# Kernel optimization log

Measured on AMD Instinct MI355X. Metric: run time of the kernel, lower is better.

## Reference

```python
import jax, jax.numpy as jnp
import numpy as np
from jax import lax

D = 512
K = 5
HID = 2 * D
EPS = 1e-5


def layernorm(x, g, b):
    mu = jnp.mean(x, axis=-1, keepdims=True)
    var = jnp.mean((x - mu) ** 2, axis=-1, keepdims=True)
    return (x - mu) * lax.rsqrt(var + EPS) * g + b


def setup_inputs() -> dict:
    key = jax.random.key(0)
    ks = jax.random.split(key, 16)
    B, T = 8, 4096
    sc = lambda fan: 1.0 / np.sqrt(fan)
    return {
        "x": jax.random.normal(ks[0], (B, T, D), jnp.float32),
        "decay_logit": jnp.zeros((D,), jnp.float32),
        "W_out": jax.random.uniform(ks[1], (D, D), jnp.float32, -sc(D), sc(D)),
        "b_out": jax.random.uniform(ks[2], (D,), jnp.float32, -sc(D), sc(D)),
        "conv_w": jax.random.uniform(ks[3], (D, 1, K), jnp.float32, -sc(K), sc(K)),
        "conv_b": jax.random.uniform(ks[4], (D,), jnp.float32, -sc(K), sc(K)),
        "ln1_g": jnp.ones((D,), jnp.float32),
        "ln1_b": jnp.zeros((D,), jnp.float32),
        "ln2_g": jnp.ones((D,), jnp.float32),
        "ln2_b": jnp.zeros((D,), jnp.float32),
        "W1": jax.random.uniform(ks[5], (HID, D), jnp.float32, -sc(D), sc(D)),
        "b1": jax.random.uniform(ks[6], (HID,), jnp.float32, -sc(D), sc(D)),
        "W2": jax.random.uniform(ks[7], (D, HID), jnp.float32, -sc(HID), sc(HID)),
        "b2": jax.random.uniform(ks[8], (D,), jnp.float32, -sc(HID), sc(HID)),
    }


def retention_core(xn, decay_logit, W_out, b_out, conv_w, conv_b):
    # xn: [B, T, D]
    B, T, _ = xn.shape
    a = jax.nn.sigmoid(decay_logit)  # [D]

    def step(s, xt):  # s, xt: [B, D]
        s = a * s + (1.0 - a) * xt
        return s, s

    s0 = jnp.zeros((B, D), xn.dtype)
    _, ss = lax.scan(step, s0, jnp.swapaxes(xn, 0, 1))  # [T, B, D]
    ss = jnp.swapaxes(ss, 0, 1)  # [B, T, D]
    y_ret = jnp.einsum("btd,ed->bte", ss, W_out) + b_out

    # depthwise conv1d, 'same' padding (K odd)
    xc = jnp.swapaxes(xn, 1, 2)  # [B, D, T]
    pad = (K - 1) // 2
    y_loc = lax.conv_general_dilated(
        xc, conv_w, window_strides=(1,), padding=[(pad, pad)],
        feature_group_count=D, dimension_numbers=("NCH", "OIH", "NCH"))
    y_loc = jnp.swapaxes(y_loc + conv_b[None, :, None], 1, 2)  # [B, T, D]
    return y_ret + y_loc


def reference(x, decay_logit, W_out, b_out, conv_w, conv_b,
              ln1_g, ln1_b, ln2_g, ln2_b, W1, b1, W2, b2):
    y = retention_core(layernorm(x, ln1_g, ln1_b),
                       decay_logit, W_out, b_out, conv_w, conv_b)
    x = x + y
    h = layernorm(x, ln2_g, ln2_b)
    h = jax.nn.gelu(jnp.einsum("btd,hd->bth", h, W1) + b1, approximate=False)
    y = jnp.einsum("bth,dh->btd", h, W2) + b2
    return x + y
```

## Files before the change

### kernel.cpp

```cpp
#include <hip/hip_runtime.h>
#include <stdint.h>

typedef unsigned short u16;

#define DIM 512
#define HIDN 1024
#define TT 4096
#define BB 8
#define MM 32768
#define CH 128
#define CL 32

__device__ __forceinline__ u16 f2bf(float f) {
  union { float f; uint32_t u; } v; v.f = f;
  uint32_t u = v.u;
  uint32_t r = u + 0x7fffu + ((u >> 16) & 1u);
  return (u16)(r >> 16);
}
__device__ __forceinline__ float bf2f(u16 h) {
  union { uint32_t u; float f; } v; v.u = ((uint32_t)h) << 16; return v.f;
}

typedef __bf16 bf16x8 __attribute__((ext_vector_type(8)));
typedef float f32x4 __attribute__((ext_vector_type(4)));

__global__ __launch_bounds__(256) void prep_kernel(
    const float* __restrict__ wout, const float* __restrict__ w1,
    const float* __restrict__ w2, const float* __restrict__ dl,
    const float* __restrict__ convw,
    u16* __restrict__ wout_h, u16* __restrict__ w1_h, u16* __restrict__ w2_h,
    float* __restrict__ a, float* __restrict__ oma, float* __restrict__ aL,
    float* __restrict__ convwT) {
  int i = blockIdx.x * 256 + threadIdx.x;
  if (i < DIM * DIM) wout_h[i] = f2bf(wout[i]);
  if (i < HIDN * DIM) { w1_h[i] = f2bf(w1[i]); w2_h[i] = f2bf(w2[i]); }
  if (i < 5 * DIM) {
    int kk = i / DIM, n = i - kk * DIM;
    convwT[i] = convw[n * 5 + kk];
  }
  if (i < DIM) {
    float av = 1.0f / (1.0f + expf(-dl[i]));
    a[i] = av; oma[i] = 1.0f - av; aL[i] = powf(av, (float)CL);
  }
}

__global__ __launch_bounds__(256) void ln_rows(
    const float* __restrict__ xin, const float* __restrict__ g,
    const float* __restrict__ bvec, u16* __restrict__ out) {
  int lane = threadIdx.x & 63, wave = threadIdx.x >> 6;
  size_t row = (size_t)blockIdx.x * 4 + wave;
  const float4* xr = (const float4*)(xin + row * DIM);
  float4 v0 = xr[lane * 2 + 0];
  float4 v1 = xr[lane * 2 + 1];
  float s1 = v0.x + v0.y + v0.z + v0.w + v1.x + v1.y + v1.z + v1.w;
  float s2 = v0.x * v0.x + v0.y * v0.y + v0.z * v0.z + v0.w * v0.w
           + v1.x * v1.x + v1.y * v1.y + v1.z * v1.z + v1.w * v1.w;
#pragma unroll
  for (int o = 1; o < 64; o <<= 1) { s1 += __shfl_xor(s1, o); s2 += __shfl_xor(s2, o); }
  float mu = s1 * (1.0f / DIM);
  float var = s2 * (1.0f / DIM) - mu * mu;
  float rs = rsqrtf(var + 1e-5f);
  const float4* gr = (const float4*)g;
  const float4* br = (const float4*)bvec;
  float4 g0 = gr[lane * 2], g1 = gr[lane * 2 + 1];
  float4 b0 = br[lane * 2], b1 = br[lane * 2 + 1];
  uint32_t p0 = (uint32_t)f2bf((v0.x - mu) * rs * g0.x + b0.x) | ((uint32_t)f2bf((v0.y - mu) * rs * g0.y + b0.y) << 16);
  uint32_t p1 = (uint32_t)f2bf((v0.z - mu) * rs * g0.z + b0.z) | ((uint32_t)f2bf((v0.w - mu) * rs * g0.w + b0.w) << 16);
  uint32_t p2 = (uint32_t)f2bf((v1.x - mu) * rs * g1.x + b1.x) | ((uint32_t)f2bf((v1.y - mu) * rs * g1.y + b1.y) << 16);
  uint32_t p3 = (uint32_t)f2bf((v1.z - mu) * rs * g1.z + b1.z) | ((uint32_t)f2bf((v1.w - mu) * rs * g1.w + b1.w) << 16);
  uint4 pk; pk.x = p0; pk.y = p1; pk.z = p2; pk.w = p3;
  ((uint4*)(out + row * DIM))[lane] = pk;
}

__global__ __launch_bounds__(256) void scan_local(
    const u16* __restrict__ xn, const float* __restrict__ a,
    const float* __restrict__ oma, float* __restrict__ carry) {
  int idx = blockIdx.x * 256 + threadIdx.x;
  int d = idx & (DIM - 1);
  int c = (idx >> 9) & (CH - 1);
  int b = idx >> 16;
  float av = a[d], om = oma[d];
  const u16* xp = xn + ((size_t)(b * TT + c * CL)) * DIM + d;
  float s = 0.f;
#pragma unroll
  for (int i = 0; i < CL; ++i)
    s = fmaf(av, s, om * bf2f(xp[(size_t)i * DIM]));
  carry[((size_t)(b * CH + c)) * DIM + d] = s;
}

__global__ __launch_bounds__(256) void scan_carry(
    const float* __restrict__ carry, const float* __restrict__ aL,
    float* __restrict__ start) {
  int idx = blockIdx.x * 256 + threadIdx.x;
  int d = idx & (DIM - 1);
  int b = idx >> 9;
  float al = aL[d];
  float s = 0.f;
#pragma unroll 8
  for (int c = 0; c < CH; ++c) {
    size_t o = ((size_t)(b * CH + c)) * DIM + d;
    start[o] = s;
    s = fmaf(al, s, carry[o]);
  }
}

__global__ __launch_bounds__(256) void scan_emit(
    const u16* __restrict__ xn, const float* __restrict__ a,
    const float* __restrict__ oma, const float* __restrict__ start,
    u16* __restrict__ ss) {
  int idx = blockIdx.x * 256 + threadIdx.x;
  int d = idx & (DIM - 1);
  int c = (idx >> 9) & (CH - 1);
  int b = idx >> 16;
  float av = a[d], om = oma[d];
  const u16* xp = xn + ((size_t)(b * TT + c * CL)) * DIM + d;
  u16* sp = ss + ((size_t)(b * TT + c * CL)) * DIM + d;
  float s = start[((size_t)(b * CH + c)) * DIM + d];
#pragma unroll
  for (int i = 0; i < CL; ++i) {
    s = fmaf(av, s, om * bf2f(xp[(size_t)i * DIM]));
    sp[(size_t)i * DIM] = f2bf(s);
  }
}

template <int Kd, int EPI>
__global__ __launch_bounds__(256) void gemm_bt(
    const u16* __restrict__ A, const u16* __restrict__ Bmat,
    const float* __restrict__ bias, const float* __restrict__ resid,
    const u16* __restrict__ xn, const float* __restrict__ convwT,
    const float* __restrict__ convb, float* __restrict__ outf,
    u16* __restrict__ outh) {
  __shared__ alignas(16) u16 sA[128 * 64];
  __shared__ alignas(16) u16 sB[128 * 64];
  const int tid = threadIdx.x;
  const int lane = tid & 63, wave = tid >> 6;
  const int wr = (wave >> 1) * 64, wc = (wave & 1) * 64;
  const int rA = lane & 15, q = lane >> 4;

  f32x4 acc[4][4];
#pragma unroll
  for (int i = 0; i < 4; i++)
#pragma unroll
    for (int j = 0; j < 4; j++) acc[i][j] = (f32x4){0.f, 0.f, 0.f, 0.f};

  const size_t rowTile = (size_t)blockIdx.y * 128;
  const size_t colTile = (size_t)blockIdx.x * 128;
  const u16* Abase = A + rowTile * Kd;
  const u16* Bbase = Bmat + colTile * Kd;

  const int lrow = lane >> 3;
  const int lslot = lane & 7;
  const int gk = ((lslot ^ lrow) & 7) * 8;

  for (int kt = 0; kt < Kd; kt += 64) {
    __syncthreads();
#pragma unroll
    for (int it = 0; it < 4; ++it) {
      const int m0 = (it * 4 + wave) * 8;
      const u16* ga = Abase + (size_t)(m0 + lrow) * Kd + kt + gk;
      const u16* gb = Bbase + (size_t)(m0 + lrow) * Kd + kt + gk;
      __builtin_amdgcn_global_load_lds(
          (const __attribute__((address_space(1))) void*)ga,
          (__attribute__((address_space(3))) void*)&sA[m0 * 64], 16, 0, 0);
      __builtin_amdgcn_global_load_lds(
          (const __attribute__((address_space(1))) void*)gb,
          (__attribute__((address_space(3))) void*)&sB[m0 * 64], 16, 0, 0);
    }
    __syncthreads();
#pragma unroll
    for (int ks = 0; ks < 2; ++ks) {
      bf16x8 af[4], bfr[4];
#pragma unroll
      for (int mi = 0; mi < 4; ++mi) {
        int r = wr + mi * 16 + rA;
        int pos = ((ks * 4 + q) ^ (r & 7));
        af[mi] = *(const bf16x8*)&sA[r * 64 + pos * 8];
      }
#pragma unroll
      for (int ni = 0; ni < 4; ++ni) {
        int r = wc + ni * 16 + rA;
        int pos = ((ks * 4 + q) ^ (r & 7));
        bfr[ni] = *(const bf16x8*)&sB[r * 64 + pos * 8];
      }
#pragma unroll
      for (int mi = 0; mi < 4; ++mi)
#pragma unroll
        for (int ni = 0; ni < 4; ++ni)
          acc[mi][ni] = __builtin_amdgcn_mfma_f32_16x16x32_bf16(bfr[ni], af[mi], acc[mi][ni], 0, 0, 0);
    }
  }

#pragma unroll
  for (int mi = 0; mi < 4; ++mi) {
    size_t m = rowTile + wr + mi * 16 + rA;
#pragma unroll
    for (int ni = 0; ni < 4; ++ni) {
      int n0 = (int)colTile + wc + ni * 16 + q * 4;
      f32x4 v = acc[mi][ni];
      float4 bv = *(const float4*)&bias[n0];
      float val0 = v[0] + bv.x, val1 = v[1] + bv.y, val2 = v[2] + bv.z, val3 = v[3] + bv.w;
      if constexpr (EPI == 0) {
        int t = (int)(m & (TT - 1));
        float4 cb = *(const float4*)&convb[n0];
        float4 rv = *(const float4*)&resid[m * DIM + n0];
        val0 += cb.x + rv.x; val1 += cb.y + rv.y; val2 += cb.z + rv.z; val3 += cb.w + rv.w;
#pragma unroll
        for (int kk = 0; kk < 5; ++kk) {
          int ttc = t + kk - 2;
          if (ttc >= 0 && ttc < TT) {
            uint2 xv = *(const uint2*)&xn[(m + (size_t)kk - 2) * DIM + n0];
            float4 wv = *(const float4*)&convwT[kk * DIM + n0];
            val0 = fmaf(wv.x, bf2f((u16)(xv.x & 0xffffu)), val0);
            val1 = fmaf(wv.y, bf2f((u16)(xv.x >> 16)), val1);
            val2 = fmaf(wv.z, bf2f((u16)(xv.y & 0xffffu)), val2);
            val3 = fmaf(wv.w, bf2f((u16)(xv.y >> 16)), val3);
          }
        }
        float4 ov; ov.x = val0; ov.y = val1; ov.z = val2; ov.w = val3;
        *(float4*)&outf[m * DIM + n0] = ov;
      } else if constexpr (EPI == 1) {
        const float isq2 = 0.70710678118654752f;
        float g0 = 0.5f * val0 * (1.0f + erff(val0 * isq2));
        float g1 = 0.5f * val1 * (1.0f + erff(val1 * isq2));
        float g2 = 0.5f * val2 * (1.0f + erff(val2 * isq2));
        float g3 = 0.5f * val3 * (1.0f + erff(val3 * isq2));
        uint2 pk;
        pk.x = (uint32_t)f2bf(g0) | ((uint32_t)f2bf(g1) << 16);
        pk.y = (uint32_t)f2bf(g2) | ((uint32_t)f2bf(g3) << 16);
        *(uint2*)&outh[m * HIDN + n0] = pk;
      } else {
        float4 rv = *(const float4*)&resid[m * DIM + n0];
        float4 ov;
        ov.x = val0 + rv.x; ov.y = val1 + rv.y; ov.z = val2 + rv.z; ov.w = val3 + rv.w;
        *(float4*)&outf[m * DIM + n0] = ov;
      }
    }
  }
}

extern "C" void kernel_launch(void* const* d_in, const int* in_sizes, int n_in,
                              void* d_out, int out_size, void* d_ws, size_t ws_size,
                              hipStream_t stream) {
  const float* x      = (const float*)d_in[0];
  const float* dl     = (const float*)d_in[1];
  const float* W_out  = (const float*)d_in[2];
  const float* b_out  = (const float*)d_in[3];
  const float* conv_w = (const float*)d_in[4];
  const float* conv_b = (const float*)d_in[5];
  const float* ln1_g  = (const float*)d_in[6];
  const float* ln1_b  = (const float*)d_in[7];
  const float* ln2_g  = (const float*)d_in[8];
  const float* ln2_b  = (const float*)d_in[9];
  const float* W1     = (const float*)d_in[10];
  const float* b1     = (const float*)d_in[11];
  const float* W2     = (const float*)d_in[12];
  const float* b2     = (const float*)d_in[13];

  char* ws = (char*)d_ws;
  u16*   wout_h = (u16*)(ws + 0);
  u16*   w1_h   = (u16*)(ws + 524288);
  u16*   w2_h   = (u16*)(ws + 1572864);
  float* a_buf  = (float*)(ws + 2621440);
  float* oma    = (float*)(ws + 2623488);
  float* aL     = (float*)(ws + 2625536);
  float* convwT = (float*)(ws + 2627584);
  float* carry  = (float*)(ws + (4u << 20));
  float* start  = (float*)(ws + 6291456);
  u16*   xn  = (u16*)(ws + (8u << 20));
  u16*   ssb = (u16*)(ws + (40u << 20));
  float* x1  = (float*)(ws + (72u << 20));
  u16*   h   = (u16*)(ws + (136u << 20));
  u16*   hg  = (u16*)(ws + (168u << 20));

  float* out = (float*)d_out;

  prep_kernel<<<2048, 256, 0, stream>>>(W_out, W1, W2, dl, conv_w, wout_h, w1_h, w2_h, a_buf, oma, aL, convwT);
  ln_rows<<<MM / 4, 256, 0, stream>>>(x, ln1_g, ln1_b, xn);
  scan_local<<<(BB * CH * DIM) / 256, 256, 0, stream>>>(xn, a_buf, oma, carry);
  scan_carry<<<(BB * DIM) / 256, 256, 0, stream>>>(carry, aL, start);
  scan_emit<<<(BB * CH * DIM) / 256, 256, 0, stream>>>(xn, a_buf, oma, start, ssb);
  gemm_bt<512, 0><<<dim3(4, MM / 128), 256, 0, stream>>>(ssb, wout_h, b_out, x, xn, convwT, conv_b, x1, nullptr);
  ln_rows<<<MM / 4, 256, 0, stream>>>(x1, ln2_g, ln2_b, h);
  gemm_bt<512, 1><<<dim3(8, MM / 128), 256, 0, stream>>>(h, w1_h, b1, nullptr, nullptr, nullptr, nullptr, nullptr, hg);
  gemm_bt<1024, 2><<<dim3(4, MM / 128), 256, 0, stream>>>(hg, w2_h, b2, x1, nullptr, nullptr, nullptr, out, nullptr);
}
```

Baseline: 434.9 us.

## Load GEMM fragments directly from global memory and vectorize scan kernels

The GEMM kernel drops its LDS staging and barriers. Each wave now loads its MFMA fragments straight from global memory into registers, double-buffered across the two k-halves, and launch bounds request 3 blocks per CU. The scan kernels each handle two channels per thread using 32-bit loads and stores, which halves the thread count. This removes LDS round-trips and syncs, but each block no longer shares loaded data through LDS, so cache traffic rises and the loads become smaller, uncoalesced-row accesses.

```diff
diff --git a/kernel.cpp b/kernel.cpp
--- a/kernel.cpp
+++ b/kernel.cpp
@@ -76,16 +76,20 @@
     const u16* __restrict__ xn, const float* __restrict__ a,
     const float* __restrict__ oma, float* __restrict__ carry) {
   int idx = blockIdx.x * 256 + threadIdx.x;
-  int d = idx & (DIM - 1);
-  int c = (idx >> 9) & (CH - 1);
-  int b = idx >> 16;
-  float av = a[d], om = oma[d];
-  const u16* xp = xn + ((size_t)(b * TT + c * CL)) * DIM + d;
-  float s = 0.f;
-#pragma unroll
-  for (int i = 0; i < CL; ++i)
-    s = fmaf(av, s, om * bf2f(xp[(size_t)i * DIM]));
-  carry[((size_t)(b * CH + c)) * DIM + d] = s;
+  int dp = (idx & 255) * 2;
+  int c = (idx >> 8) & (CH - 1);
+  int b = idx >> 15;
+  float a0 = a[dp], a1 = a[dp + 1], o0 = oma[dp], o1 = oma[dp + 1];
+  const uint32_t* xp = (const uint32_t*)(xn + ((size_t)(b * TT + c * CL)) * DIM + dp);
+  float s0 = 0.f, s1 = 0.f;
+#pragma unroll
+  for (int i = 0; i < CL; ++i) {
+    uint32_t u = xp[(size_t)i * (DIM / 2)];
+    s0 = fmaf(a0, s0, o0 * bf2f((u16)(u & 0xffffu)));
+    s1 = fmaf(a1, s1, o1 * bf2f((u16)(u >> 16)));
+  }
+  float2 cv; cv.x = s0; cv.y = s1;
+  *(float2*)&carry[((size_t)(b * CH + c)) * DIM + dp] = cv;
 }
 
 __global__ __launch_bounds__(256) void scan_carry(
@@ -109,85 +113,74 @@
     const float* __restrict__ oma, const float* __restrict__ start,
     u16* __restrict__ ss) {
   int idx = blockIdx.x * 256 + threadIdx.x;
-  int d = idx & (DIM - 1);
-  int c = (idx >> 9) & (CH - 1);
-  int b = idx >> 16;
-  float av = a[d], om = oma[d];
-  const u16* xp = xn + ((size_t)(b * TT + c * CL)) * DIM + d;
-  u16* sp = ss + ((size_t)(b * TT + c * CL)) * DIM + d;
-  float s = start[((size_t)(b * CH + c)) * DIM + d];
+  int dp = (idx & 255) * 2;
+  int c = (idx >> 8) & (CH - 1);
+  int b = idx >> 15;
+  float a0 = a[dp], a1 = a[dp + 1], o0 = oma[dp], o1 = oma[dp + 1];
+  const uint32_t* xp = (const uint32_t*)(xn + ((size_t)(b * TT + c * CL)) * DIM + dp);
+  uint32_t* sp = (uint32_t*)(ss + ((size_t)(b * TT + c * CL)) * DIM + dp);
+  float2 st = *(const float2*)&start[((size_t)(b * CH + c)) * DIM + dp];
+  float s0 = st.x, s1 = st.y;
 #pragma unroll
   for (int i = 0; i < CL; ++i) {
-    s = fmaf(av, s, om * bf2f(xp[(size_t)i * DIM]));
-    sp[(size_t)i * DIM] = f2bf(s);
+    uint32_t u = xp[(size_t)i * (DIM / 2)];
+    s0 = fmaf(a0, s0, o0 * bf2f((u16)(u & 0xffffu)));
+    s1 = fmaf(a1, s1, o1 * bf2f((u16)(u >> 16)));
+    sp[(size_t)i * (DIM / 2)] = (uint32_t)f2bf(s0) | ((uint32_t)f2bf(s1) << 16);
   }
 }
 
 template <int Kd, int EPI>
-__global__ __launch_bounds__(256) void gemm_bt(
+__global__ __launch_bounds__(256, 3) void gemm_bt(
     const u16* __restrict__ A, const u16* __restrict__ Bmat,
     const float* __restrict__ bias, const float* __restrict__ resid,
     const u16* __restrict__ xn, const float* __restrict__ convwT,
     const float* __restrict__ convb, float* __restrict__ outf,
     u16* __restrict__ outh) {
-  __shared__ alignas(16) u16 sA[128 * 64];
-  __shared__ alignas(16) u16 sB[128 * 64];
   const int tid = threadIdx.x;
   const int lane = tid & 63, wave = tid >> 6;
   const int wr = (wave >> 1) * 64, wc = (wave & 1) * 64;
   const int rA = lane & 15, q = lane >> 4;
 
-  f32x4 acc[4][4];
-#pragma unroll
-  for (int i = 0; i < 4; i++)
-#pragma unroll
-    for (int j = 0; j < 4; j++) acc[i][j] = (f32x4){0.f, 0.f, 0.f, 0.f};
-
   const size_t rowTile = (size_t)blockIdx.y * 128;
   const size_t colTile = (size_t)blockIdx.x * 128;
-  const u16* Abase = A + rowTile * Kd;
-  const u16* Bbase = Bmat + colTile * Kd;
-
-  const int lrow = lane >> 3;
-  const int lslot = lane & 7;
-  const int gk = ((lslot ^ lrow) & 7) * 8;
-
+  const u16* pA = A + (rowTile + wr + rA) * Kd + q * 8;
+  const u16* pB = Bmat + (colTile + wc + rA) * Kd + q * 8;
+
+  f32x4 acc[4][4];
+#pragma unroll
+  for (int i = 0; i < 4; i++)
+#pragma unroll
+    for (int j = 0; j < 4; j++) acc[i][j] = (f32x4){0.f, 0.f, 0.f, 0.f};
+
+  bf16x8 a0[4], b0[4], a1[4], b1[4];
+#pragma unroll
+  for (int mi = 0; mi < 4; ++mi) a0[mi] = *(const bf16x8*)(pA + (size_t)mi * 16 * Kd);
+#pragma unroll
+  for (int ni = 0; ni < 4; ++ni) b0[ni] = *(const bf16x8*)(pB + (size_t)ni * 16 * Kd);
+
+#pragma unroll 1
   for (int kt = 0; kt < Kd; kt += 64) {
-    __syncthreads();
-#pragma unroll
-    for (int it = 0; it < 4; ++it) {
-      const int m0 = (it * 4 + wave) * 8;
-      const u16* ga = Abase + (size_t)(m0 + lrow) * Kd + kt + gk;
-      const u16* gb = Bbase + (size_t)(m0 + lrow) * Kd + kt + gk;
-      __builtin_amdgcn_global_load_lds(
-          (const __attribute__((address_space(1))) void*)ga,
-          (__attribute__((address_space(3))) void*)&sA[m0 * 64], 16, 0, 0);
-      __builtin_amdgcn_global_load_lds(
-          (const __attribute__((address_space(1))) void*)gb,
-          (__attribute__((address_space(3))) void*)&sB[m0 * 64], 16, 0, 0);
+#pragma unroll
+    for (int mi = 0; mi < 4; ++mi) a1[mi] = *(const bf16x8*)(pA + (size_t)mi * 16 * Kd + kt + 32);
+#pragma unroll
+    for (int ni = 0; ni < 4; ++ni) b1[ni] = *(const bf16x8*)(pB + (size_t)ni * 16 * Kd + kt + 32);
+#pragma unroll
+    for (int mi = 0; mi < 4; ++mi)
+#pragma unroll
+      for (int ni = 0; ni < 4; ++ni)
+        acc[mi][ni] = __builtin_amdgcn_mfma_f32_16x16x32_bf16(b0[ni], a0[mi], acc[mi][ni], 0, 0, 0);
+    if (kt + 64 < Kd) {
+#pragma unroll
+      for (int mi = 0; mi < 4; ++mi) a0[mi] = *(const bf16x8*)(pA + (size_t)mi * 16 * Kd + kt + 64);
+#pragma unroll
+      for (int ni = 0; ni < 4; ++ni) b0[ni] = *(const bf16x8*)(pB + (size_t)ni * 16 * Kd + kt + 64);
     }
-    __syncthreads();
-#pragma unroll
-    for (int ks = 0; ks < 2; ++ks) {
-      bf16x8 af[4], bfr[4];
-#pragma unroll
-      for (int mi = 0; mi < 4; ++mi) {
-        int r = wr + mi * 16 + rA;
-        int pos = ((ks * 4 + q) ^ (r & 7));
-        af[mi] = *(const bf16x8*)&sA[r * 64 + pos * 8];
-      }
-#pragma unroll
-      for (int ni = 0; ni < 4; ++ni) {
-        int r = wc + ni * 16 + rA;
-        int pos = ((ks * 4 + q) ^ (r & 7));
-        bfr[ni] = *(const bf16x8*)&sB[r * 64 + pos * 8];
-      }
-#pragma unroll
-      for (int mi = 0; mi < 4; ++mi)
-#pragma unroll
-        for (int ni = 0; ni < 4; ++ni)
-          acc[mi][ni] = __builtin_amdgcn_mfma_f32_16x16x32_bf16(bfr[ni], af[mi], acc[mi][ni], 0, 0, 0);
-    }
+#pragma unroll
+    for (int mi = 0; mi < 4; ++mi)
+#pragma unroll
+      for (int ni = 0; ni < 4; ++ni)
+        acc[mi][ni] = __builtin_amdgcn_mfma_f32_16x16x32_bf16(b1[ni], a1[mi], acc[mi][ni], 0, 0, 0);
   }
 
 #pragma unroll
@@ -276,9 +269,9 @@
 
   prep_kernel<<<2048, 256, 0, stream>>>(W_out, W1, W2, dl, conv_w, wout_h, w1_h, w2_h, a_buf, oma, aL, convwT);
   ln_rows<<<MM / 4, 256, 0, stream>>>(x, ln1_g, ln1_b, xn);
-  scan_local<<<(BB * CH * DIM) / 256, 256, 0, stream>>>(xn, a_buf, oma, carry);
+  scan_local<<<(BB * CH * DIM / 2) / 256, 256, 0, stream>>>(xn, a_buf, oma, carry);
   scan_carry<<<(BB * DIM) / 256, 256, 0, stream>>>(carry, aL, start);
-  scan_emit<<<(BB * CH * DIM) / 256, 256, 0, stream>>>(xn, a_buf, oma, start, ssb);
+  scan_emit<<<(BB * CH * DIM / 2) / 256, 256, 0, stream>>>(xn, a_buf, oma, start, ssb);
   gemm_bt<512, 0><<<dim3(4, MM / 128), 256, 0, stream>>>(ssb, wout_h, b_out, x, xn, convwT, conv_b, x1, nullptr);
   ln_rows<<<MM / 4, 256, 0, stream>>>(x1, ln2_g, ln2_b, h);
   gemm_bt<512, 1><<<dim3(8, MM / 128), 256, 0, stream>>>(h, w1_h, b1, nullptr, nullptr, nullptr, nullptr, nullptr, hg);
```

New measurement: 574.5 us. 1.32x slower.
